# Kernel tuning notes

Measured on AMD Instinct MI355X. Metric: run time of the kernel, lower is better.

The kernel has to match this reference:

```python
import jax, jax.numpy as jnp
import numpy as np

DIN = 2048
DOUT = 2048
NUM_HEADS = 16
HEAD_DIM = DIN // NUM_HEADS  # 128
BLOCK_SIZE = 2048
ROPE_THETA = 10000.0


def precompute_freqs(block_size, head_dim):
    inv_freq = 1.0 / (ROPE_THETA ** (jnp.arange(0, head_dim, 2, dtype=jnp.float32) / head_dim))
    t = jnp.arange(block_size, dtype=jnp.float32)
    freqs = jnp.outer(t, inv_freq)  # [S, head_dim//2]
    return jnp.cos(freqs), jnp.sin(freqs)


def apply_rotary_emb(x, cos, sin):
    # x: [B, S, H, D]; cos/sin: [S, D//2]
    xr = x.reshape(*x.shape[:-1], -1, 2)  # pairs of consecutive dims (complex view)
    x1, x2 = xr[..., 0], xr[..., 1]
    c = cos[None, :, None, :]
    s = sin[None, :, None, :]
    o1 = x1 * c - x2 * s
    o2 = x1 * s + x2 * c
    return jnp.stack([o1, o2], axis=-1).reshape(x.shape)


def setup_inputs() -> dict:
    key = jax.random.key(0)
    k1, k2, k3 = jax.random.split(key, 3)
    x = jax.random.normal(k1, (2, 2048, DIN), dtype=jnp.float32)
    Wqkv = jax.random.normal(k2, (DIN, 3 * DOUT), dtype=jnp.float32) * (DIN ** -0.5)
    Wproj = jax.random.normal(k3, (DIN, DOUT), dtype=jnp.float32) * (DIN ** -0.5)
    return {"x": x, "Wqkv": Wqkv, "Wproj": Wproj}


def reference(x, Wqkv, Wproj):
    B, S, _ = x.shape
    cos, sin = precompute_freqs(BLOCK_SIZE, HEAD_DIM)
    cos, sin = cos[:S], sin[:S]
    qkv = x @ Wqkv  # [B, S, 3*DOUT]
    q, k, v = jnp.split(qkv, 3, axis=-1)
    q = q.reshape(B, S, NUM_HEADS, HEAD_DIM)
    k = k.reshape(B, S, NUM_HEADS, HEAD_DIM)
    v = v.reshape(B, S, NUM_HEADS, HEAD_DIM)
    q = apply_rotary_emb(q, cos, sin)
    k = apply_rotary_emb(k, cos, sin)
    # causal SDPA with scale 1/sqrt(head_dim)
    scale = HEAD_DIM ** -0.5
    scores = jnp.einsum('bqhd,bkhd->bhqk', q, k) * scale
    causal = jnp.tril(jnp.ones((S, S), dtype=bool))
    scores = jnp.where(causal[None, None], scores, jnp.finfo(scores.dtype).min)
    attn = jax.nn.softmax(scores, axis=-1)
    y = jnp.einsum('bhqk,bkhd->bqhd', attn, v).reshape(B, S, DOUT)
    return y @ Wproj
```

## Files before the change

kernel.cpp:

```cpp
#include <hip/hip_runtime.h>

#define DIN 2048
#define NH 16
#define DH 128
#define SEQ 2048
#define BB 2
#define N3 6144
#define MM 4096

typedef __bf16 bf16;
typedef __attribute__((ext_vector_type(8))) __bf16 bf16x8;
typedef __attribute__((ext_vector_type(4))) __bf16 bf16x4;
typedef __attribute__((ext_vector_type(4))) float f32x4;

__device__ __forceinline__ f32x4 mfma16(bf16x8 a, bf16x8 b, f32x4 c) {
  return __builtin_amdgcn_mfma_f32_16x16x32_bf16(a, b, c, 0, 0, 0);
}

__device__ __forceinline__ void async16(const void* g, void* l) {
  __builtin_amdgcn_global_load_lds((const __attribute__((address_space(1))) void*)g,
                                   (__attribute__((address_space(3))) void*)l, 16, 0, 0);
}

__global__ void sniff_k(const unsigned short* __restrict__ x, int* __restrict__ flag) {
  __shared__ int cnt;
  if (threadIdx.x == 0) cnt = 0;
  __syncthreads();
  unsigned short u = x[threadIdx.x * 2];
  int e = (u >> 7) & 0xff;
  if (e >= 108 && e <= 140) atomicAdd(&cnt, 1);
  __syncthreads();
  if (threadIdx.x == 0) *flag = (cnt >= 128) ? 1 : 0;
}

__global__ __launch_bounds__(256) void cast_x_k(const void* __restrict__ in, bf16* __restrict__ out,
                                                const int* __restrict__ flag) {
  size_t i = ((size_t)blockIdx.x * 256 + threadIdx.x) * 8;
  if (*flag) {
    *(bf16x8*)(out + i) = *(const bf16x8*)((const bf16*)in + i);
  } else {
    const float* f = (const float*)in;
    bf16x8 v;
    for (int j = 0; j < 8; j++) v[j] = (bf16)f[i + j];
    *(bf16x8*)(out + i) = v;
  }
}

__global__ __launch_bounds__(256) void cast_wT_k(const void* __restrict__ in, bf16* __restrict__ out,
                                                 const int* __restrict__ flag, int R, int C) {
  __shared__ float t[32][33];
  int c0 = blockIdx.x * 32, r0 = blockIdx.y * 32;
  int tx = threadIdx.x & 31, ty = threadIdx.x >> 5;
  bool isb = *flag != 0;
  for (int j = 0; j < 4; j++) {
    int r = ty + j * 8;
    size_t idx = (size_t)(r0 + r) * C + c0 + tx;
    float v = isb ? (float)((const bf16*)in)[idx] : ((const float*)in)[idx];
    t[r][tx] = v;
  }
  __syncthreads();
  for (int j = 0; j < 4; j++) {
    int c = ty + j * 8;
    out[(size_t)(c0 + c) * R + r0 + tx] = (bf16)t[tx][c];
  }
}

__global__ __launch_bounds__(256) void gemm_qkv_k(const bf16* __restrict__ A, const bf16* __restrict__ BT,
                                                  bf16* __restrict__ Qb, bf16* __restrict__ Kb,
                                                  bf16* __restrict__ Vb) {
  __shared__ __align__(16) bf16 As[128 * 32];
  __shared__ __align__(16) bf16 Bs[128 * 32];
  const int K = DIN;
  int m0 = blockIdx.y * 128, n0 = blockIdx.x * 128;
  int tid = threadIdx.x, w = tid >> 6, l = tid & 63;
  int l15 = l & 15, quad = l >> 4;
  int wm = (w & 1) * 64, wn = (w >> 1) * 64;
  f32x4 zero = {0.f, 0.f, 0.f, 0.f};
  f32x4 acc[4][4];
  for (int i = 0; i < 4; i++)
    for (int j = 0; j < 4; j++) acc[i][j] = zero;
  const bf16* Ag = A + (size_t)(m0 + w * 32 + (l >> 2)) * K + (l & 3) * 8;
  const bf16* Bg = BT + (size_t)(n0 + w * 32 + (l >> 2)) * K + (l & 3) * 8;
  bf16* AsW = As + (w * 32) * 32;
  bf16* BsW = Bs + (w * 32) * 32;
  for (int k0 = 0; k0 < K; k0 += 32) {
    __syncthreads();
    async16(Ag + k0, AsW);
    async16(Ag + k0 + 16 * K, AsW + 16 * 32);
    async16(Bg + k0, BsW);
    async16(Bg + k0 + 16 * K, BsW + 16 * 32);
    __syncthreads();
    bf16x8 af[4], bfv[4];
    for (int i = 0; i < 4; i++) af[i] = *(const bf16x8*)&As[(wm + i * 16 + l15) * 32 + quad * 8];
    for (int j = 0; j < 4; j++) bfv[j] = *(const bf16x8*)&Bs[(wn + j * 16 + l15) * 32 + quad * 8];
    for (int i = 0; i < 4; i++)
      for (int j = 0; j < 4; j++) acc[i][j] = mfma16(af[i], bfv[j], acc[i][j]);
  }
  for (int j = 0; j < 4; j++) {
    int col = n0 + wn + j * 16 + l15;
    int part = col >> 11, cw = col & 2047;
    int h = cw >> 7, d = cw & 127;
    bf16* dst = (part == 0) ? Qb : ((part == 1) ? Kb : Vb);
    for (int i = 0; i < 4; i++) {
      int mrow = m0 + wm + i * 16 + quad * 4;
      for (int r = 0; r < 4; r++) {
        int m = mrow + r;
        int b = m >> 11, s = m & 2047;
        int dd = (part == 1) ? (((((d >> 3) ^ (s & 7)) << 3)) | (d & 7)) : d;
        dst[(((size_t)(b * NH + h)) * SEQ + s) * DH + dd] = (bf16)acc[i][j][r];
      }
    }
  }
}

__global__ __launch_bounds__(256) void rope_k(bf16* __restrict__ Qb, bf16* __restrict__ Kb) {
  int i = blockIdx.x * 256 + threadIdx.x;
  int d2 = i & 63;
  int s = (i >> 6) & 2047;
  int bh = i >> 17;
  int dl = 2 * d2;
  float invf = expf(-9.210340371976184f * (float)dl * (1.0f / 128.0f));
  float ang = (float)s * invf;
  float sn, cs;
  sincosf(ang, &sn, &cs);
  size_t row = ((size_t)bh * SEQ + s) * DH;
  const float scale = 0.08838834764831845f * 1.4426950408889634f;
  size_t qb = row + dl;
  float q1 = (float)Qb[qb], q2 = (float)Qb[qb + 1];
  Qb[qb] = (bf16)((q1 * cs - q2 * sn) * scale);
  Qb[qb + 1] = (bf16)((q1 * sn + q2 * cs) * scale);
  size_t kb = row + ((((dl >> 3) ^ (s & 7)) << 3) | (dl & 7));
  float k1 = (float)Kb[kb], k2 = (float)Kb[kb + 1];
  Kb[kb] = (bf16)(k1 * cs - k2 * sn);
  Kb[kb + 1] = (bf16)(k1 * sn + k2 * cs);
}

__global__ __launch_bounds__(256) void transpose_v_k(const bf16* __restrict__ V, bf16* __restrict__ Vt) {
  __shared__ float t[32][33];
  int s0 = blockIdx.x * 32, d0 = blockIdx.y * 32;
  int bh = blockIdx.z;
  const bf16* Vp = V + (size_t)bh * SEQ * DH;
  bf16* Vo = Vt + (size_t)bh * DH * SEQ;
  int tx = threadIdx.x & 31, ty = threadIdx.x >> 5;
  for (int j = 0; j < 4; j++)
    t[ty + j * 8][tx] = (float)Vp[(size_t)(s0 + ty + j * 8) * DH + d0 + tx];
  __syncthreads();
  for (int j = 0; j < 4; j++) {
    int dh = d0 + ty + j * 8;
    int s = s0 + tx;
    int sl = s & 63;
    int col = (s & ~63) | ((((sl >> 3) ^ (dh & 7)) << 3) | (sl & 7));
    Vo[(size_t)dh * SEQ + col] = (bf16)t[tx][ty + j * 8];
  }
}

__global__ __launch_bounds__(256, 1) void attn_k(const bf16* __restrict__ Qb, const bf16* __restrict__ Kb,
                                                 const bf16* __restrict__ Vt, bf16* __restrict__ Yb) {
  __shared__ __align__(16) bf16 Ks[2][64 * 128];
  __shared__ __align__(16) bf16 Vs[2][128 * 64];
  __shared__ __align__(16) bf16 Pl[4][32 * 72];
  int bh = blockIdx.x;
  int slot = blockIdx.y;
  int w = threadIdx.x >> 6, l = threadIdx.x & 63;
  int l15 = l & 15, quad = l >> 4;
  const bf16* Qp = Qb + (size_t)bh * SEQ * DH;
  const bf16* Kp = Kb + (size_t)bh * SEQ * DH;
  const bf16* Vp = Vt + (size_t)bh * DH * SEQ;
  int b = bh >> 4, h = bh & 15;
  f32x4 zero = {0.f, 0.f, 0.f, 0.f};
  bf16* P = &Pl[w][0];

  auto stage = [&](int it, int buf) {
    const char* gk = (const char*)Kp + (size_t)it * 16384 + w * 4096 + l * 16;
    char* lk = (char*)&Ks[buf][0] + w * 4096;
    for (int i = 0; i < 4; i++) async16(gk + i * 1024, lk + i * 1024);
    const char* gv = (const char*)Vp + (size_t)it * 128 + (size_t)(w * 32 + (l >> 3)) * (SEQ * 2) + (l & 7) * 16;
    char* lv = (char*)&Vs[buf][0] + w * 32 * 128;
    for (int i = 0; i < 4; i++) async16(gv + (size_t)i * 8 * (SEQ * 2), lv + i * 1024);
  };

  int tiles[2] = {15 - slot, slot};
  for (int half = 0; half < 2; half++) {
    int tile = tiles[half];
    int q0 = tile * 128;
    int qw = q0 + w * 32;
    bf16x8 qf[2][4];
    for (int rb = 0; rb < 2; rb++)
      for (int kc = 0; kc < 4; kc++)
        qf[rb][kc] = *(const bf16x8*)&Qp[(size_t)(qw + rb * 16 + l15) * DH + kc * 32 + quad * 8];
    f32x4 o[2][8];
    for (int rb = 0; rb < 2; rb++)
      for (int ns = 0; ns < 8; ns++) o[rb][ns] = zero;
    float mprev[2] = {-1e30f, -1e30f}, lsum[2] = {0.f, 0.f};
    int nkt = 2 * tile + 2;

    stage(0, 0);
    __syncthreads();
    for (int it = 0; it < nkt; it++) {
      int buf = it & 1;
      if (it + 1 < nkt) stage(it + 1, buf ^ 1);
      int k0 = it * 64;
      bool act1 = (k0 <= qw + 31);
      bool act0 = (k0 <= qw + 15);
      if (act1) {
        f32x4 st0[4], st1[4];
        for (int ns = 0; ns < 4; ns++) { st0[ns] = zero; st1[ns] = zero; }
        for (int kc = 0; kc < 4; kc++)
          for (int ns = 0; ns < 4; ns++) {
            bf16x8 kf = *(const bf16x8*)&Ks[buf][(ns * 16 + l15) * 128 + (((kc * 4 + quad) ^ (l15 & 7)) << 3)];
            st1[ns] = mfma16(kf, qf[1][kc], st1[ns]);
            if (act0) st0[ns] = mfma16(kf, qf[0][kc], st0[ns]);
          }
        for (int rb = 0; rb < 2; rb++) {
          if (rb == 0 && !act0) continue;
          f32x4* st = (rb == 0) ? st0 : st1;
          int qq = qw + rb * 16 + l15;
          if (k0 + 63 > qw + rb * 16) {
            for (int ns = 0; ns < 4; ns++) {
              int kk = k0 + ns * 16 + quad * 4;
              for (int r = 0; r < 4; r++)
                if (kk + r > qq) st[ns][r] = -1e30f;
            }
          }
          float pm = -1e30f;
          for (int ns = 0; ns < 4; ns++)
            for (int r = 0; r < 4; r++) pm = fmaxf(pm, st[ns][r]);
          pm = fmaxf(pm, __shfl_xor(pm, 16, 64));
          pm = fmaxf(pm, __shfl_xor(pm, 32, 64));
          float mnew = fmaxf(mprev[rb], pm);
          float al = exp2f(mprev[rb] - mnew);
          mprev[rb] = mnew;
          float ps = 0.f;
          for (int ns = 0; ns < 4; ns++)
            for (int r = 0; r < 4; r++) {
              float e = exp2f(st[ns][r] - mnew);
              st[ns][r] = e;
              ps += e;
            }
          ps += __shfl_xor(ps, 16, 64);
          ps += __shfl_xor(ps, 32, 64);
          lsum[rb] = lsum[rb] * al + ps;
          for (int ns = 0; ns < 8; ns++) o[rb][ns] *= al;
          for (int ns = 0; ns < 4; ns++) {
            bf16x4 pk;
            for (int r = 0; r < 4; r++) pk[r] = (bf16)st[ns][r];
            *(bf16x4*)&P[(rb * 16 + l15) * 72 + ns * 16 + quad * 4] = pk;
          }
        }
        asm volatile("s_waitcnt lgkmcnt(0)" ::: "memory");
        bf16x8 pa0[2], pa1[2];
        for (int kc = 0; kc < 2; kc++)
          pa1[kc] = *(const bf16x8*)&P[(16 + l15) * 72 + kc * 32 + quad * 8];
        if (act0)
          for (int kc = 0; kc < 2; kc++)
            pa0[kc] = *(const bf16x8*)&P[l15 * 72 + kc * 32 + quad * 8];
        for (int ns = 0; ns < 8; ns++)
          for (int kc = 0; kc < 2; kc++) {
            bf16x8 vf = *(const bf16x8*)&Vs[buf][(ns * 16 + l15) * 64 + (((kc * 4 + quad) ^ (l15 & 7)) << 3)];
            o[1][ns] = mfma16(vf, pa1[kc], o[1][ns]);
            if (act0) o[0][ns] = mfma16(vf, pa0[kc], o[0][ns]);
          }
      }
      __syncthreads();
    }
    for (int rb = 0; rb < 2; rb++) {
      float inv = 1.0f / lsum[rb];
      int q = qw + rb * 16 + l15;
      size_t base = ((size_t)(b * SEQ + q)) * DIN + h * DH + quad * 4;
      for (int ns = 0; ns < 8; ns++) {
        bf16x4 pk;
        for (int r = 0; r < 4; r++) pk[r] = (bf16)(o[rb][ns][r] * inv);
        *(bf16x4*)&Yb[base + ns * 16] = pk;
      }
    }
  }
}

__global__ __launch_bounds__(256) void gemm_proj_k(const bf16* __restrict__ A, const bf16* __restrict__ BT,
                                                   void* __restrict__ out, const int* __restrict__ flag) {
  __shared__ __align__(16) bf16 As[128 * 32];
  __shared__ __align__(16) bf16 Bs[128 * 32];
  const int K = DIN;
  int m0 = blockIdx.y * 128, n0 = blockIdx.x * 128;
  int tid = threadIdx.x, w = tid >> 6, l = tid & 63;
  int l15 = l & 15, quad = l >> 4;
  int wm = (w & 1) * 64, wn = (w >> 1) * 64;
  bool obf = *flag != 0;
  f32x4 zero = {0.f, 0.f, 0.f, 0.f};
  f32x4 acc[4][4];
  for (int i = 0; i < 4; i++)
    for (int j = 0; j < 4; j++) acc[i][j] = zero;
  const bf16* Ag = A + (size_t)(m0 + w * 32 + (l >> 2)) * K + (l & 3) * 8;
  const bf16* Bg = BT + (size_t)(n0 + w * 32 + (l >> 2)) * K + (l & 3) * 8;
  bf16* AsW = As + (w * 32) * 32;
  bf16* BsW = Bs + (w * 32) * 32;
  for (int k0 = 0; k0 < K; k0 += 32) {
    __syncthreads();
    async16(Ag + k0, AsW);
    async16(Ag + k0 + 16 * K, AsW + 16 * 32);
    async16(Bg + k0, BsW);
    async16(Bg + k0 + 16 * K, BsW + 16 * 32);
    __syncthreads();
    bf16x8 af[4], bfv[4];
    for (int i = 0; i < 4; i++) af[i] = *(const bf16x8*)&As[(wm + i * 16 + l15) * 32 + quad * 8];
    for (int j = 0; j < 4; j++) bfv[j] = *(const bf16x8*)&Bs[(wn + j * 16 + l15) * 32 + quad * 8];
    for (int i = 0; i < 4; i++)
      for (int j = 0; j < 4; j++) acc[i][j] = mfma16(af[i], bfv[j], acc[i][j]);
  }
  for (int j = 0; j < 4; j++) {
    int col = n0 + wn + j * 16 + l15;
    for (int i = 0; i < 4; i++) {
      int mrow = m0 + wm + i * 16 + quad * 4;
      for (int r = 0; r < 4; r++) {
        size_t idx = (size_t)(mrow + r) * DIN + col;
        float v = acc[i][j][r];
        if (obf)
          ((bf16*)out)[idx] = (bf16)v;
        else
          ((float*)out)[idx] = v;
      }
    }
  }
}

extern "C" void kernel_launch(void* const* d_in, const int* in_sizes, int n_in,
                              void* d_out, int out_size, void* d_ws, size_t ws_size,
                              hipStream_t stream) {
  char* ws = (char*)d_ws;
  int* flag = (int*)ws;
  bf16* Xb = (bf16*)(ws + 256);
  bf16* WqkvT = (bf16*)(ws + 256 + 16777216);
  bf16* WprojT = (bf16*)(ws + 256 + 16777216 + 25165824);
  bf16* Qb = (bf16*)(ws + 256 + 16777216 + 25165824 + 8388608);
  bf16* Kb = Qb + (size_t)MM * DIN;
  bf16* Vb = Kb + (size_t)MM * DIN;
  bf16* Vt = Vb + (size_t)MM * DIN;
  bf16* Yb = Xb;

  sniff_k<<<1, 256, 0, stream>>>((const unsigned short*)d_in[0], flag);
  cast_x_k<<<4096, 256, 0, stream>>>(d_in[0], Xb, flag);
  cast_wT_k<<<dim3(192, 64), 256, 0, stream>>>(d_in[1], WqkvT, flag, DIN, N3);
  cast_wT_k<<<dim3(64, 64), 256, 0, stream>>>(d_in[2], WprojT, flag, DIN, DIN);
  gemm_qkv_k<<<dim3(48, 32), 256, 0, stream>>>(Xb, WqkvT, Qb, Kb, Vb);
  rope_k<<<16384, 256, 0, stream>>>(Qb, Kb);
  transpose_v_k<<<dim3(64, 4, 32), 256, 0, stream>>>(Vb, Vt);
  attn_k<<<dim3(32, 8), 256, 0, stream>>>(Qb, Kb, Vt, Yb);
  gemm_proj_k<<<dim3(16, 32), 256, 0, stream>>>(Yb, WprojT, d_out, flag);
}
```

Baseline: 455.4 us.

## Shrink attention query tile to 64 rows and double grid for occupancy

The attention kernel now gives each wave 16 query rows instead of 32, so a block covers a 64-row query tile. The grid doubles to 512 blocks with two blocks per CU allowed, and causal tiles are still paired (31-slot, slot) for load balance. This cuts register pressure, removes the per-row-block activity branching and raises occupancy and parallelism. In exchange each K/V tile loaded into LDS is reused by half as many query rows, which doubles K/V traffic.

```diff
diff --git a/kernel.cpp b/kernel.cpp
--- a/kernel.cpp
+++ b/kernel.cpp
@@ -154,11 +154,11 @@
   }
 }
 
-__global__ __launch_bounds__(256, 1) void attn_k(const bf16* __restrict__ Qb, const bf16* __restrict__ Kb,
+__global__ __launch_bounds__(256, 2) void attn_k(const bf16* __restrict__ Qb, const bf16* __restrict__ Kb,
                                                  const bf16* __restrict__ Vt, bf16* __restrict__ Yb) {
   __shared__ __align__(16) bf16 Ks[2][64 * 128];
   __shared__ __align__(16) bf16 Vs[2][128 * 64];
-  __shared__ __align__(16) bf16 Pl[4][32 * 72];
+  __shared__ __align__(16) bf16 Pl[4][16 * 76];
   int bh = blockIdx.x;
   int slot = blockIdx.y;
   int w = threadIdx.x >> 6, l = threadIdx.x & 63;
@@ -179,20 +179,17 @@
     for (int i = 0; i < 4; i++) async16(gv + (size_t)i * 8 * (SEQ * 2), lv + i * 1024);
   };
 
-  int tiles[2] = {15 - slot, slot};
+  int tiles[2] = {31 - slot, slot};
   for (int half = 0; half < 2; half++) {
     int tile = tiles[half];
-    int q0 = tile * 128;
-    int qw = q0 + w * 32;
-    bf16x8 qf[2][4];
-    for (int rb = 0; rb < 2; rb++)
-      for (int kc = 0; kc < 4; kc++)
-        qf[rb][kc] = *(const bf16x8*)&Qp[(size_t)(qw + rb * 16 + l15) * DH + kc * 32 + quad * 8];
-    f32x4 o[2][8];
-    for (int rb = 0; rb < 2; rb++)
-      for (int ns = 0; ns < 8; ns++) o[rb][ns] = zero;
-    float mprev[2] = {-1e30f, -1e30f}, lsum[2] = {0.f, 0.f};
-    int nkt = 2 * tile + 2;
+    int qw = tile * 64 + w * 16;
+    bf16x8 qf[4];
+    for (int kc = 0; kc < 4; kc++)
+      qf[kc] = *(const bf16x8*)&Qp[(size_t)(qw + l15) * DH + kc * 32 + quad * 8];
+    f32x4 o[8];
+    for (int ns = 0; ns < 8; ns++) o[ns] = zero;
+    float mprev = -1e30f, lsum = 0.f;
+    int nkt = tile + 1;
 
     stage(0, 0);
     __syncthreads();
@@ -200,78 +197,63 @@
       int buf = it & 1;
       if (it + 1 < nkt) stage(it + 1, buf ^ 1);
       int k0 = it * 64;
-      bool act1 = (k0 <= qw + 31);
-      bool act0 = (k0 <= qw + 15);
-      if (act1) {
-        f32x4 st0[4], st1[4];
-        for (int ns = 0; ns < 4; ns++) { st0[ns] = zero; st1[ns] = zero; }
-        for (int kc = 0; kc < 4; kc++)
-          for (int ns = 0; ns < 4; ns++) {
-            bf16x8 kf = *(const bf16x8*)&Ks[buf][(ns * 16 + l15) * 128 + (((kc * 4 + quad) ^ (l15 & 7)) << 3)];
-            st1[ns] = mfma16(kf, qf[1][kc], st1[ns]);
-            if (act0) st0[ns] = mfma16(kf, qf[0][kc], st0[ns]);
-          }
-        for (int rb = 0; rb < 2; rb++) {
-          if (rb == 0 && !act0) continue;
-          f32x4* st = (rb == 0) ? st0 : st1;
-          int qq = qw + rb * 16 + l15;
-          if (k0 + 63 > qw + rb * 16) {
-            for (int ns = 0; ns < 4; ns++) {
-              int kk = k0 + ns * 16 + quad * 4;
-              for (int r = 0; r < 4; r++)
-                if (kk + r > qq) st[ns][r] = -1e30f;
-            }
-          }
-          float pm = -1e30f;
-          for (int ns = 0; ns < 4; ns++)
-            for (int r = 0; r < 4; r++) pm = fmaxf(pm, st[ns][r]);
-          pm = fmaxf(pm, __shfl_xor(pm, 16, 64));
-          pm = fmaxf(pm, __shfl_xor(pm, 32, 64));
-          float mnew = fmaxf(mprev[rb], pm);
-          float al = exp2f(mprev[rb] - mnew);
-          mprev[rb] = mnew;
-          float ps = 0.f;
-          for (int ns = 0; ns < 4; ns++)
-            for (int r = 0; r < 4; r++) {
-              float e = exp2f(st[ns][r] - mnew);
-              st[ns][r] = e;
-              ps += e;
-            }
-          ps += __shfl_xor(ps, 16, 64);
-          ps += __shfl_xor(ps, 32, 64);
-          lsum[rb] = lsum[rb] * al + ps;
-          for (int ns = 0; ns < 8; ns++) o[rb][ns] *= al;
-          for (int ns = 0; ns < 4; ns++) {
-            bf16x4 pk;
-            for (int r = 0; r < 4; r++) pk[r] = (bf16)st[ns][r];
-            *(bf16x4*)&P[(rb * 16 + l15) * 72 + ns * 16 + quad * 4] = pk;
-          }
+      f32x4 st[4];
+      for (int ns = 0; ns < 4; ns++) st[ns] = zero;
+      for (int kc = 0; kc < 4; kc++)
+        for (int ns = 0; ns < 4; ns++) {
+          bf16x8 kf = *(const bf16x8*)&Ks[buf][(ns * 16 + l15) * 128 + (((kc * 4 + quad) ^ (l15 & 7)) << 3)];
+          st[ns] = mfma16(kf, qf[kc], st[ns]);
         }
-        asm volatile("s_waitcnt lgkmcnt(0)" ::: "memory");
-        bf16x8 pa0[2], pa1[2];
-        for (int kc = 0; kc < 2; kc++)
-          pa1[kc] = *(const bf16x8*)&P[(16 + l15) * 72 + kc * 32 + quad * 8];
-        if (act0)
-          for (int kc = 0; kc < 2; kc++)
-            pa0[kc] = *(const bf16x8*)&P[l15 * 72 + kc * 32 + quad * 8];
-        for (int ns = 0; ns < 8; ns++)
-          for (int kc = 0; kc < 2; kc++) {
-            bf16x8 vf = *(const bf16x8*)&Vs[buf][(ns * 16 + l15) * 64 + (((kc * 4 + quad) ^ (l15 & 7)) << 3)];
-            o[1][ns] = mfma16(vf, pa1[kc], o[1][ns]);
-            if (act0) o[0][ns] = mfma16(vf, pa0[kc], o[0][ns]);
-          }
+      int qq = qw + l15;
+      if (k0 + 63 > qw) {
+        for (int ns = 0; ns < 4; ns++) {
+          int kk = k0 + ns * 16 + quad * 4;
+          for (int r = 0; r < 4; r++)
+            if (kk + r > qq) st[ns][r] = -1e30f;
+        }
       }
+      float pm = -1e30f;
+      for (int ns = 0; ns < 4; ns++)
+        for (int r = 0; r < 4; r++) pm = fmaxf(pm, st[ns][r]);
+      pm = fmaxf(pm, __shfl_xor(pm, 16, 64));
+      pm = fmaxf(pm, __shfl_xor(pm, 32, 64));
+      float mnew = fmaxf(mprev, pm);
+      float al = exp2f(mprev - mnew);
+      mprev = mnew;
+      float ps = 0.f;
+      for (int ns = 0; ns < 4; ns++)
+        for (int r = 0; r < 4; r++) {
+          float e = exp2f(st[ns][r] - mnew);
+          st[ns][r] = e;
+          ps += e;
+        }
+      ps += __shfl_xor(ps, 16, 64);
+      ps += __shfl_xor(ps, 32, 64);
+      lsum = lsum * al + ps;
+      for (int ns = 0; ns < 8; ns++) o[ns] *= al;
+      for (int ns = 0; ns < 4; ns++) {
+        bf16x4 pk;
+        for (int r = 0; r < 4; r++) pk[r] = (bf16)st[ns][r];
+        *(bf16x4*)&P[l15 * 76 + ns * 16 + quad * 4] = pk;
+      }
+      asm volatile("s_waitcnt lgkmcnt(0)" ::: "memory");
+      bf16x8 pa[2];
+      for (int kc = 0; kc < 2; kc++)
+        pa[kc] = *(const bf16x8*)&P[l15 * 76 + kc * 32 + quad * 8];
+      for (int ns = 0; ns < 8; ns++)
+        for (int kc = 0; kc < 2; kc++) {
+          bf16x8 vf = *(const bf16x8*)&Vs[buf][(ns * 16 + l15) * 64 + (((kc * 4 + quad) ^ (l15 & 7)) << 3)];
+          o[ns] = mfma16(vf, pa[kc], o[ns]);
+        }
       __syncthreads();
     }
-    for (int rb = 0; rb < 2; rb++) {
-      float inv = 1.0f / lsum[rb];
-      int q = qw + rb * 16 + l15;
-      size_t base = ((size_t)(b * SEQ + q)) * DIN + h * DH + quad * 4;
-      for (int ns = 0; ns < 8; ns++) {
-        bf16x4 pk;
-        for (int r = 0; r < 4; r++) pk[r] = (bf16)(o[rb][ns][r] * inv);
-        *(bf16x4*)&Yb[base + ns * 16] = pk;
-      }
+    float inv = 1.0f / lsum;
+    int q = qw + l15;
+    size_t base = ((size_t)(b * SEQ + q)) * DIN + h * DH + quad * 4;
+    for (int ns = 0; ns < 8; ns++) {
+      bf16x4 pk;
+      for (int r = 0; r < 4; r++) pk[r] = (bf16)(o[ns][r] * inv);
+      *(bf16x4*)&Yb[base + ns * 16] = pk;
     }
   }
 }
@@ -344,6 +326,6 @@
   gemm_qkv_k<<<dim3(48, 32), 256, 0, stream>>>(Xb, WqkvT, Qb, Kb, Vb);
   rope_k<<<16384, 256, 0, stream>>>(Qb, Kb);
   transpose_v_k<<<dim3(64, 4, 32), 256, 0, stream>>>(Vb, Vt);
-  attn_k<<<dim3(32, 8), 256, 0, stream>>>(Qb, Kb, Vt, Yb);
+  attn_k<<<dim3(32, 16), 256, 0, stream>>>(Qb, Kb, Vt, Yb);
   gemm_proj_k<<<dim3(16, 32), 256, 0, stream>>>(Yb, WprojT, d_out, flag);
 }
```

After: 415.2 us. 1.1x faster.
